# Kernel optimization log

Measured on AMD Instinct MI355X. Metric: run time of the kernel, lower is better.

The kernel has to match this reference:

```python
import jax, jax.numpy as jnp
import numpy as np

B, S, D, H = 4, 2048, 1024, 16
HD = D // H


def setup_inputs() -> dict:
    key = jax.random.key(0)
    ks = jax.random.split(key, 12)
    def lin(k):
        return jax.random.normal(k, (D, D), dtype=jnp.float32) * 0.02
    return {
        "query": jax.random.normal(ks[0], (B, S, D), dtype=jnp.float32),
        "key": jax.random.normal(ks[1], (B, S, D), dtype=jnp.float32),
        "value": jax.random.normal(ks[2], (B, S, D), dtype=jnp.float32),
        "Wq": lin(ks[3]), "bq": jnp.zeros((D,), jnp.float32),
        "Wk": lin(ks[4]), "bk": jnp.zeros((D,), jnp.float32),
        "Wv": lin(ks[5]), "bv": jnp.zeros((D,), jnp.float32),
        "Wo": lin(ks[6]), "bo": jnp.zeros((D,), jnp.float32),
        "pad_mask": jnp.ones((B, S), dtype=jnp.int32),
    }


def reference(query, key, value, Wq, bq, Wk, bk, Wv, bv, Wo, bo, pad_mask):
    # torch nn.Linear convention: y = x @ W.T + b
    Q = query @ Wq.T + bq   # [B,Sq,D]
    K = key @ Wk.T + bk     # [B,Sk,D]
    V = value @ Wv.T + bv
    Sq, Sk = Q.shape[1], K.shape[1]
    Q = Q.reshape(B, Sq, H, HD).transpose(0, 2, 1, 3)  # [B,H,Sq,hd]
    K = K.reshape(B, Sk, H, HD).transpose(0, 2, 1, 3)
    V = V.reshape(B, Sk, H, HD).transpose(0, 2, 1, 3)
    scores = jnp.einsum('bhqd,bhkd->bhqk', Q, K) / jnp.sqrt(jnp.float32(HD))
    # causal (lookahead) mask
    causal = jnp.tril(jnp.ones((Sq, Sk), dtype=bool))
    scores = jnp.where(causal[None, None], scores, -jnp.inf)
    # pad mask broadcast [B,1,Sq,1]
    pm = (pad_mask[:, None, :, None] != 0)
    scores = jnp.where(pm, scores, -jnp.inf)
    attn = jax.nn.softmax(scores, axis=-1)
    out = jnp.einsum('bhqk,bhkd->bhqd', attn, V)  # [B,H,Sq,hd]
    out = out.transpose(0, 2, 1, 3).reshape(B, Sq, D)
    return out @ Wo.T + bo
```

## Files before the change

kernel.cpp:

```cpp
#include <hip/hip_runtime.h>
#include <hip/hip_bf16.h>
#include <stdint.h>

typedef __attribute__((ext_vector_type(8))) short bf16x8;
typedef __attribute__((ext_vector_type(4))) float f32x4;

#define HD 64
#define NH 16
#define SEQ 2048
#define DM 1024

#define GLDS16(gp, lp)                                                      \
    __builtin_amdgcn_global_load_lds(                                       \
        (const __attribute__((address_space(1))) void*)(gp),                \
        (__attribute__((address_space(3))) void*)(lp), 16, 0, 0)

__device__ inline bf16x8 cvt8(const float* __restrict__ p) {
    float4 a = *(const float4*)p;
    float4 b = *(const float4*)(p + 4);
    union { bf16x8 v; __hip_bfloat16 e[8]; } u;
    u.e[0] = __float2bfloat16(a.x); u.e[1] = __float2bfloat16(a.y);
    u.e[2] = __float2bfloat16(a.z); u.e[3] = __float2bfloat16(a.w);
    u.e[4] = __float2bfloat16(b.x); u.e[5] = __float2bfloat16(b.y);
    u.e[6] = __float2bfloat16(b.z); u.e[7] = __float2bfloat16(b.w);
    return u.v;
}

__global__ __launch_bounds__(256)
void cvtw(const float* __restrict__ a, const float* __restrict__ b,
          const float* __restrict__ c, const float* __restrict__ d,
          __hip_bfloat16* __restrict__ o)
{
    int g = blockIdx.x * 256 + threadIdx.x;
    int t = g * 4;
    const float* src;
    switch (t >> 20) {
        case 0: src = a; break;
        case 1: src = b; break;
        case 2: src = c; break;
        default: src = d; break;
    }
    float4 v = *(const float4*)(src + (t & 0xFFFFF));
    union { ushort4 u; __hip_bfloat16 e[4]; } w;
    w.e[0] = __float2bfloat16(v.x); w.e[1] = __float2bfloat16(v.y);
    w.e[2] = __float2bfloat16(v.z); w.e[3] = __float2bfloat16(v.w);
    *(ushort4*)(o + t) = w.u;
}

__global__ __launch_bounds__(256)
void cvtx(const float* __restrict__ src, __hip_bfloat16* __restrict__ dst)
{
    int t = (blockIdx.x * 256 + threadIdx.x) * 8;
    *(bf16x8*)(dst + t) = cvt8(src + t);
}

template<int OMODE>
__global__ __launch_bounds__(256)
void gemm16(const __hip_bfloat16* __restrict__ X,
            const __hip_bfloat16* __restrict__ Wb,
            const float* __restrict__ bias,
            void* __restrict__ Yv,
            int M, int N, int K, float scale)
{
    __shared__ alignas(16) __hip_bfloat16 As[128 * 32];
    __shared__ alignas(16) __hip_bfloat16 Bs[128 * 32];

    const int tid  = threadIdx.x;
    const int lane = tid & 63;
    const int wv   = tid >> 6;
    const int quad = lane >> 4;
    const int l15  = lane & 15;
    const int wm   = (wv >> 1) * 64;
    const int wn   = (wv & 1) * 64;

    int bx = blockIdx.x, by = blockIdx.y;
    if (gridDim.x == 8 && gridDim.y == 64) {
        int lin = by * 8 + bx;
        bx = lin >> 6;
        by = ((lin & 7) << 3) | ((lin >> 3) & 7);
    }
    const int m0 = by * 128;
    const int n0 = bx * 128;

    f32x4 acc[4][4] = {};

    for (int k0 = 0; k0 < K; k0 += 32) {
        #pragma unroll
        for (int it = 0; it < 2; ++it) {
            int c = tid + it * 256;
            int row = c >> 2, cg = c & 3;
            GLDS16(&X[(size_t)(m0 + row) * K + k0 + cg * 8],
                   (char*)As + (size_t)c * 16);
            GLDS16(&Wb[(size_t)(n0 + row) * K + k0 + cg * 8],
                   (char*)Bs + (size_t)c * 16);
        }
        __syncthreads();

        bf16x8 af[4], bfr[4];
        #pragma unroll
        for (int i = 0; i < 4; ++i)
            af[i] = *(const bf16x8*)(&As[(wm + i * 16 + l15) * 32 + quad * 8]);
        #pragma unroll
        for (int j = 0; j < 4; ++j)
            bfr[j] = *(const bf16x8*)(&Bs[(wn + j * 16 + l15) * 32 + quad * 8]);

        #pragma unroll
        for (int i = 0; i < 4; ++i)
            #pragma unroll
            for (int j = 0; j < 4; ++j)
                acc[i][j] = __builtin_amdgcn_mfma_f32_16x16x32_bf16(
                    af[i], bfr[j], acc[i][j], 0, 0, 0);
        __syncthreads();
    }

    #pragma unroll
    for (int j = 0; j < 4; ++j) {
        int n = n0 + wn + j * 16 + l15;
        float bv = bias[n];
        int h = n >> 6, hd = n & 63;
        #pragma unroll
        for (int i = 0; i < 4; ++i) {
            int mb = m0 + wm + i * 16 + quad * 4;
            if (OMODE == 0) {
                __hip_bfloat16* Y = (__hip_bfloat16*)Yv;
                #pragma unroll
                for (int r = 0; r < 4; ++r) {
                    int m = mb + r;
                    int b = m >> 11, s = m & 2047;
                    Y[((size_t)(b * NH + h) * SEQ + s) * HD + hd] =
                        __float2bfloat16((acc[i][j][r] + bv) * scale);
                }
            } else if (OMODE == 2) {
                __hip_bfloat16* Y = (__hip_bfloat16*)Yv;
                int b = mb >> 11, s = mb & 2047;
                union { ushort4 u; __hip_bfloat16 e[4]; } w;
                #pragma unroll
                for (int r = 0; r < 4; ++r)
                    w.e[r] = __float2bfloat16(acc[i][j][r] + bv);
                *(ushort4*)(&Y[((size_t)(b * NH + h) * HD + hd) * SEQ + s]) = w.u;
            } else {
                float* Y = (float*)Yv;
                #pragma unroll
                for (int r = 0; r < 4; ++r)
                    Y[(size_t)(mb + r) * N + n] = acc[i][j][r] + bv;
            }
        }
    }
}

__device__ __forceinline__ unsigned pk2(float lo, float hi) {
    union { unsigned u; __hip_bfloat16 h[2]; } w;
    w.h[0] = __float2bfloat16(lo);
    w.h[1] = __float2bfloat16(hi);
    return w.u;
}

__device__ __forceinline__ void swap16(unsigned& a, unsigned& b) {
    asm("v_permlane16_swap_b32 %0, %1" : "+v"(a), "+v"(b));
}

__device__ __forceinline__ void attn_tile(
    const bf16x8 (&aqs)[2], f32x4 (&os)[4], f32x4& o5,
    const __hip_bfloat16* __restrict__ K_, const __hip_bfloat16* __restrict__ V_,
    const bf16x8 ones, int kv0, int qabs, bool diag,
    int quad, int l15, int sw, int qp)
{
    f32x4 sv[4];
    #pragma unroll
    for (int jk = 0; jk < 4; ++jk) {
        f32x4 s = {};
        #pragma unroll
        for (int ks = 0; ks < 2; ++ks) {
            bf16x8 kf = *(const bf16x8*)(
                &K_[(jk * 16 + l15) * 64 + (((ks * 4 + quad) ^ sw) * 8)]);
            s = __builtin_amdgcn_mfma_f32_16x16x32_bf16(kf, aqs[ks], s, 0, 0, 0);
        }
        sv[jk] = s;
    }
    unsigned P[4][2];
    #pragma unroll
    for (int jk = 0; jk < 4; ++jk) {
        int kvb = kv0 + jk * 16 + quad * 4;
        #pragma unroll
        for (int h = 0; h < 2; ++h) {
            float e0 = __builtin_amdgcn_exp2f(sv[jk][2 * h]);
            float e1 = __builtin_amdgcn_exp2f(sv[jk][2 * h + 1]);
            if (diag) {
                e0 = (kvb + 2 * h     <= qabs) ? e0 : 0.f;
                e1 = (kvb + 2 * h + 1 <= qabs) ? e1 : 0.f;
            }
            P[jk][h] = pk2(e0, e1);
        }
    }
    swap16(P[0][0], P[1][0]);
    swap16(P[0][1], P[1][1]);
    swap16(P[2][0], P[3][0]);
    swap16(P[2][1], P[3][1]);
    union { bf16x8 v; unsigned u[4]; } fa0, fa1;
    fa0.u[0] = P[0][0]; fa0.u[1] = P[0][1]; fa0.u[2] = P[1][0]; fa0.u[3] = P[1][1];
    fa1.u[0] = P[2][0]; fa1.u[1] = P[2][1]; fa1.u[2] = P[3][0]; fa1.u[3] = P[3][1];
    #pragma unroll
    for (int jn = 0; jn < 4; ++jn) {
        bf16x8 vb0 = *(const bf16x8*)(
            &V_[(jn * 16 + l15) * 64 + ((qp ^ sw) * 8)]);
        bf16x8 vb1 = *(const bf16x8*)(
            &V_[(jn * 16 + l15) * 64 + (((4 + qp) ^ sw) * 8)]);
        os[jn] = __builtin_amdgcn_mfma_f32_16x16x32_bf16(fa0.v, vb0, os[jn], 0, 0, 0);
        os[jn] = __builtin_amdgcn_mfma_f32_16x16x32_bf16(fa1.v, vb1, os[jn], 0, 0, 0);
    }
    o5 = __builtin_amdgcn_mfma_f32_16x16x32_bf16(fa0.v, ones, o5, 0, 0, 0);
    o5 = __builtin_amdgcn_mfma_f32_16x16x32_bf16(fa1.v, ones, o5, 0, 0, 0);
}

__global__ __launch_bounds__(256, 4)
void attn(const __hip_bfloat16* __restrict__ Qh,
          const __hip_bfloat16* __restrict__ Kh,
          const __hip_bfloat16* __restrict__ Vt,
          __hip_bfloat16* __restrict__ O)
{
    __shared__ alignas(16) __hip_bfloat16 Ks[2][64 * 64];
    __shared__ alignas(16) __hip_bfloat16 VsT[2][64 * 64];

    const int tid  = threadIdx.x;
    const int lane = tid & 63;
    const int wv   = tid >> 6;
    const int quad = lane >> 4;
    const int l15  = lane & 15;
    const int bh   = blockIdx.y;
    const int b    = bh >> 4;
    const int h    = bh & 15;
    const int p    = blockIdx.x;
    const int sa   = p;
    const int sb   = 31 - p;
    const int sw   = l15 & 7;
    const int qp   = ((quad & 1) << 1) | (quad >> 1);

    const __hip_bfloat16* Qp  = Qh + (size_t)bh * SEQ * HD;
    const __hip_bfloat16* Kp  = Kh + (size_t)bh * SEQ * HD;
    const __hip_bfloat16* Vtp = Vt + (size_t)bh * HD * SEQ;

    union { bf16x8 v; short e[8]; } onesu;
    #pragma unroll
    for (int i = 0; i < 8; ++i) onesu.e[i] = (short)0x3F80;
    const bf16x8 ones = onesu.v;

    bf16x8 aq[2][2];
    #pragma unroll
    for (int s = 0; s < 2; ++s) {
        int qb = (s ? sb : sa) * 64;
        #pragma unroll
        for (int ks = 0; ks < 2; ++ks)
            aq[s][ks] = *(const bf16x8*)(
                &Qp[(size_t)(qb + wv * 16 + l15) * HD + ks * 32 + quad * 8]);
    }

    f32x4 o[2][4] = {};
    f32x4 o5[2]   = {};

    const int srow = tid >> 3;
    const int scg  = (tid & 7) ^ (srow & 7);
    const __hip_bfloat16* kSrc = Kp + (size_t)srow * HD + scg * 8;
    const __hip_bfloat16* vSrc = Vtp + (size_t)srow * SEQ + scg * 8;
    char* kDst0 = (char*)Ks[0]  + tid * 16;
    char* vDst0 = (char*)VsT[0] + tid * 16;

    auto STAGE = [&](int bufi, int kv0) {
        size_t kadv = (size_t)kv0 * HD;
        int boff = bufi * 8192;
        GLDS16(kSrc + kadv,           kDst0 + boff);
        GLDS16(kSrc + kadv + 32 * HD, kDst0 + boff + 4096);
        GLDS16(vSrc + kv0,            vDst0 + boff);
        GLDS16(vSrc + kv0 + 32 * SEQ, vDst0 + boff + 4096);
    };

    const int nit = sa + sb + 2;

    STAGE(0, 0);

    for (int i = 0; i < nit; ++i) {
        __syncthreads();

        int ni = i + 1;
        if (ni < nit) {
            int t2 = (ni <= sb) ? ni : ni - sb - 1;
            STAGE(ni & 1, t2 * 64);
        }

        const int cb    = i & 1;
        const bool isB  = (i <= sb);
        const int t     = isB ? i : i - sb - 1;
        const int strip = isB ? sb : sa;
        const int kv0   = t * 64;
        const bool diag = (t == strip);
        const int qabs  = strip * 64 + wv * 16 + l15;

        const __hip_bfloat16* K_ = Ks[cb];
        const __hip_bfloat16* V_ = VsT[cb];

        if (isB)
            attn_tile(aq[1], o[1], o5[1], K_, V_, ones, kv0, qabs, diag, quad, l15, sw, qp);
        else
            attn_tile(aq[0], o[0], o5[0], K_, V_, ones, kv0, qabs, diag, quad, l15, sw, qp);
    }

    #pragma unroll
    for (int s = 0; s < 2; ++s) {
        int strip = s ? sb : sa;
        float inv[4];
        #pragma unroll
        for (int r = 0; r < 4; ++r)
            inv[r] = 1.0f / o5[s][r];
        #pragma unroll
        for (int jn = 0; jn < 4; ++jn) {
            #pragma unroll
            for (int r = 0; r < 4; ++r) {
                int q = strip * 64 + wv * 16 + quad * 4 + r;
                O[((size_t)(b * SEQ + q)) * DM + h * HD + jn * 16 + l15] =
                    __float2bfloat16(o[s][jn][r] * inv[r]);
            }
        }
    }
}

extern "C" void kernel_launch(void* const* d_in, const int* in_sizes, int n_in,
                              void* d_out, int out_size, void* d_ws, size_t ws_size,
                              hipStream_t stream)
{
    const float* query = (const float*)d_in[0];
    const float* key_  = (const float*)d_in[1];
    const float* value = (const float*)d_in[2];
    const float* Wq = (const float*)d_in[3];
    const float* bq = (const float*)d_in[4];
    const float* Wk = (const float*)d_in[5];
    const float* bk = (const float*)d_in[6];
    const float* Wv = (const float*)d_in[7];
    const float* bv = (const float*)d_in[8];
    const float* Wo = (const float*)d_in[9];
    const float* bo = (const float*)d_in[10];

    const size_t WSZ = (size_t)1024 * 1024;
    const size_t MAT = (size_t)8192 * 1024;
    __hip_bfloat16* wb = (__hip_bfloat16*)d_ws;
    __hip_bfloat16* Qh = wb + 4 * WSZ;
    __hip_bfloat16* Kh = Qh + MAT;
    __hip_bfloat16* Vt = Kh + MAT;
    __hip_bfloat16* Oa = Vt + MAT;
    float* out = (float*)d_out;

    const float SC = 0.18033688f;

    dim3 bb(256);
    dim3 gg(8, 64);
    cvtw<<<4096, bb, 0, stream>>>(Wq, Wk, Wv, Wo, wb);
    cvtx<<<4096, bb, 0, stream>>>(query, Oa);
    gemm16<0><<<gg, bb, 0, stream>>>(Oa, wb,           bq, Qh, 8192, 1024, 1024, SC);
    cvtx<<<4096, bb, 0, stream>>>(key_, Oa);
    gemm16<0><<<gg, bb, 0, stream>>>(Oa, wb + WSZ,     bk, Kh, 8192, 1024, 1024, 1.0f);
    cvtx<<<4096, bb, 0, stream>>>(value, Oa);
    gemm16<2><<<gg, bb, 0, stream>>>(Oa, wb + 2 * WSZ, bv, Vt, 8192, 1024, 1024, 1.0f);
    attn<<<dim3(16, 64), bb, 0, stream>>>(Qh, Kh, Vt, Oa);
    gemm16<1><<<gg, bb, 0, stream>>>(Oa, wb + 3 * WSZ, bo, out, 8192, 1024, 1024, 1.0f);
}
```

Before: 363.9 us.

## Fuse fp32-to-bf16 conversion into GEMM tile loads and prioritize attention MFMAs

Removes the separate weight and activation conversion kernels. The GEMMs now load fp32 tiles straight into LDS with an XOR swizzle and convert to bf16 when building fragments. This drops the extra global writes and reads of bf16 copies and four kernel launches, but doubles the LDS footprint and global traffic per tile and adds conversion work inside the inner loop. It also adds s_setprio around the MFMA sections in the attention tile and swizzles the bf16 A tile for the output projection.

```diff
diff --git a/kernel.cpp b/kernel.cpp
--- a/kernel.cpp
+++ b/kernel.cpp
@@ -15,55 +15,30 @@
         (const __attribute__((address_space(1))) void*)(gp),                \
         (__attribute__((address_space(3))) void*)(lp), 16, 0, 0)
 
-__device__ inline bf16x8 cvt8(const float* __restrict__ p) {
-    float4 a = *(const float4*)p;
-    float4 b = *(const float4*)(p + 4);
-    union { bf16x8 v; __hip_bfloat16 e[8]; } u;
-    u.e[0] = __float2bfloat16(a.x); u.e[1] = __float2bfloat16(a.y);
-    u.e[2] = __float2bfloat16(a.z); u.e[3] = __float2bfloat16(a.w);
-    u.e[4] = __float2bfloat16(b.x); u.e[5] = __float2bfloat16(b.y);
-    u.e[6] = __float2bfloat16(b.z); u.e[7] = __float2bfloat16(b.w);
-    return u.v;
-}
-
-__global__ __launch_bounds__(256)
-void cvtw(const float* __restrict__ a, const float* __restrict__ b,
-          const float* __restrict__ c, const float* __restrict__ d,
-          __hip_bfloat16* __restrict__ o)
+__device__ __forceinline__ unsigned pk2(float lo, float hi) {
+    union { unsigned u; __hip_bfloat16 h[2]; } w;
+    w.h[0] = __float2bfloat16(lo);
+    w.h[1] = __float2bfloat16(hi);
+    return w.u;
+}
+
+__device__ __forceinline__ bf16x8 ldfrag_f32(const char* base, int row, int quad) {
+    f32x4 a = *(const f32x4*)(base + (size_t)row * 128 + (((2 * quad)     ^ (row & 7)) * 16));
+    f32x4 b = *(const f32x4*)(base + (size_t)row * 128 + (((2 * quad + 1) ^ (row & 7)) * 16));
+    union { bf16x8 v; unsigned u[4]; } w;
+    w.u[0] = pk2(a[0], a[1]); w.u[1] = pk2(a[2], a[3]);
+    w.u[2] = pk2(b[0], b[1]); w.u[3] = pk2(b[2], b[3]);
+    return w.v;
+}
+
+template<int OMODE, bool XF32>
+__global__ __launch_bounds__(256, 4)
+void gemmf(const void* __restrict__ Xv, const float* __restrict__ Wf,
+           const float* __restrict__ bias, void* __restrict__ Yv,
+           int M, int N, int K, float scale)
 {
-    int g = blockIdx.x * 256 + threadIdx.x;
-    int t = g * 4;
-    const float* src;
-    switch (t >> 20) {
-        case 0: src = a; break;
-        case 1: src = b; break;
-        case 2: src = c; break;
-        default: src = d; break;
-    }
-    float4 v = *(const float4*)(src + (t & 0xFFFFF));
-    union { ushort4 u; __hip_bfloat16 e[4]; } w;
-    w.e[0] = __float2bfloat16(v.x); w.e[1] = __float2bfloat16(v.y);
-    w.e[2] = __float2bfloat16(v.z); w.e[3] = __float2bfloat16(v.w);
-    *(ushort4*)(o + t) = w.u;
-}
-
-__global__ __launch_bounds__(256)
-void cvtx(const float* __restrict__ src, __hip_bfloat16* __restrict__ dst)
-{
-    int t = (blockIdx.x * 256 + threadIdx.x) * 8;
-    *(bf16x8*)(dst + t) = cvt8(src + t);
-}
-
-template<int OMODE>
-__global__ __launch_bounds__(256)
-void gemm16(const __hip_bfloat16* __restrict__ X,
-            const __hip_bfloat16* __restrict__ Wb,
-            const float* __restrict__ bias,
-            void* __restrict__ Yv,
-            int M, int N, int K, float scale)
-{
-    __shared__ alignas(16) __hip_bfloat16 As[128 * 32];
-    __shared__ alignas(16) __hip_bfloat16 Bs[128 * 32];
+    __shared__ alignas(16) char As[16384];
+    __shared__ alignas(16) char Bs[16384];
 
     const int tid  = threadIdx.x;
     const int lane = tid & 63;
@@ -86,23 +61,46 @@
 
     for (int k0 = 0; k0 < K; k0 += 32) {
         #pragma unroll
-        for (int it = 0; it < 2; ++it) {
-            int c = tid + it * 256;
-            int row = c >> 2, cg = c & 3;
-            GLDS16(&X[(size_t)(m0 + row) * K + k0 + cg * 8],
-                   (char*)As + (size_t)c * 16);
-            GLDS16(&Wb[(size_t)(n0 + row) * K + k0 + cg * 8],
-                   (char*)Bs + (size_t)c * 16);
+        for (int it = 0; it < 4; ++it) {
+            int g = tid + it * 256;
+            int row = g >> 3, cl = (g & 7) ^ (row & 7);
+            GLDS16(&Wf[(size_t)(n0 + row) * K + k0 + cl * 4],
+                   Bs + (size_t)g * 16);
+        }
+        if (XF32) {
+            const float* X = (const float*)Xv;
+            #pragma unroll
+            for (int it = 0; it < 4; ++it) {
+                int g = tid + it * 256;
+                int row = g >> 3, cl = (g & 7) ^ (row & 7);
+                GLDS16(&X[(size_t)(m0 + row) * K + k0 + cl * 4],
+                       As + (size_t)g * 16);
+            }
+        } else {
+            const __hip_bfloat16* X = (const __hip_bfloat16*)Xv;
+            #pragma unroll
+            for (int it = 0; it < 2; ++it) {
+                int g = tid + it * 256;
+                int row = g >> 2, cl = (g & 3) ^ (row & 3);
+                GLDS16(&X[(size_t)(m0 + row) * K + k0 + cl * 8],
+                       As + (size_t)g * 16);
+            }
         }
         __syncthreads();
 
         bf16x8 af[4], bfr[4];
         #pragma unroll
-        for (int i = 0; i < 4; ++i)
-            af[i] = *(const bf16x8*)(&As[(wm + i * 16 + l15) * 32 + quad * 8]);
+        for (int i = 0; i < 4; ++i) {
+            int row = wm + i * 16 + l15;
+            if (XF32) {
+                af[i] = ldfrag_f32(As, row, quad);
+            } else {
+                af[i] = *(const bf16x8*)(As + (size_t)row * 64 + ((quad ^ (row & 3)) * 16));
+            }
+        }
         #pragma unroll
         for (int j = 0; j < 4; ++j)
-            bfr[j] = *(const bf16x8*)(&Bs[(wn + j * 16 + l15) * 32 + quad * 8]);
+            bfr[j] = ldfrag_f32(Bs, wn + j * 16 + l15, quad);
 
         #pragma unroll
         for (int i = 0; i < 4; ++i)
@@ -148,13 +146,6 @@
     }
 }
 
-__device__ __forceinline__ unsigned pk2(float lo, float hi) {
-    union { unsigned u; __hip_bfloat16 h[2]; } w;
-    w.h[0] = __float2bfloat16(lo);
-    w.h[1] = __float2bfloat16(hi);
-    return w.u;
-}
-
 __device__ __forceinline__ void swap16(unsigned& a, unsigned& b) {
     asm("v_permlane16_swap_b32 %0, %1" : "+v"(a), "+v"(b));
 }
@@ -166,6 +157,7 @@
     int quad, int l15, int sw, int qp)
 {
     f32x4 sv[4];
+    __builtin_amdgcn_s_setprio(1);
     #pragma unroll
     for (int jk = 0; jk < 4; ++jk) {
         f32x4 s = {};
@@ -177,6 +169,7 @@
         }
         sv[jk] = s;
     }
+    __builtin_amdgcn_s_setprio(0);
     unsigned P[4][2];
     #pragma unroll
     for (int jk = 0; jk < 4; ++jk) {
@@ -199,6 +192,7 @@
     union { bf16x8 v; unsigned u[4]; } fa0, fa1;
     fa0.u[0] = P[0][0]; fa0.u[1] = P[0][1]; fa0.u[2] = P[1][0]; fa0.u[3] = P[1][1];
     fa1.u[0] = P[2][0]; fa1.u[1] = P[2][1]; fa1.u[2] = P[3][0]; fa1.u[3] = P[3][1];
+    __builtin_amdgcn_s_setprio(1);
     #pragma unroll
     for (int jn = 0; jn < 4; ++jn) {
         bf16x8 vb0 = *(const bf16x8*)(
@@ -210,6 +204,7 @@
     }
     o5 = __builtin_amdgcn_mfma_f32_16x16x32_bf16(fa0.v, ones, o5, 0, 0, 0);
     o5 = __builtin_amdgcn_mfma_f32_16x16x32_bf16(fa1.v, ones, o5, 0, 0, 0);
+    __builtin_amdgcn_s_setprio(0);
 }
 
 __global__ __launch_bounds__(256, 4)
@@ -338,10 +333,8 @@
     const float* Wo = (const float*)d_in[9];
     const float* bo = (const float*)d_in[10];
 
-    const size_t WSZ = (size_t)1024 * 1024;
     const size_t MAT = (size_t)8192 * 1024;
-    __hip_bfloat16* wb = (__hip_bfloat16*)d_ws;
-    __hip_bfloat16* Qh = wb + 4 * WSZ;
+    __hip_bfloat16* Qh = (__hip_bfloat16*)d_ws;
     __hip_bfloat16* Kh = Qh + MAT;
     __hip_bfloat16* Vt = Kh + MAT;
     __hip_bfloat16* Oa = Vt + MAT;
@@ -351,13 +344,9 @@
 
     dim3 bb(256);
     dim3 gg(8, 64);
-    cvtw<<<4096, bb, 0, stream>>>(Wq, Wk, Wv, Wo, wb);
-    cvtx<<<4096, bb, 0, stream>>>(query, Oa);
-    gemm16<0><<<gg, bb, 0, stream>>>(Oa, wb,           bq, Qh, 8192, 1024, 1024, SC);
-    cvtx<<<4096, bb, 0, stream>>>(key_, Oa);
-    gemm16<0><<<gg, bb, 0, stream>>>(Oa, wb + WSZ,     bk, Kh, 8192, 1024, 1024, 1.0f);
-    cvtx<<<4096, bb, 0, stream>>>(value, Oa);
-    gemm16<2><<<gg, bb, 0, stream>>>(Oa, wb + 2 * WSZ, bv, Vt, 8192, 1024, 1024, 1.0f);
+    gemmf<0, true ><<<gg, bb, 0, stream>>>(query, Wq, bq, Qh, 8192, 1024, 1024, SC);
+    gemmf<0, true ><<<gg, bb, 0, stream>>>(key_,  Wk, bk, Kh, 8192, 1024, 1024, 1.0f);
+    gemmf<2, true ><<<gg, bb, 0, stream>>>(value, Wv, bv, Vt, 8192, 1024, 1024, 1.0f);
     attn<<<dim3(16, 64), bb, 0, stream>>>(Qh, Kh, Vt, Oa);
-    gemm16<1><<<gg, bb, 0, stream>>>(Oa, wb + 3 * WSZ, bo, out, 8192, 1024, 1024, 1.0f);
-}
+    gemmf<1, false><<<gg, bb, 0, stream>>>(Oa, Wo, bo, out, 8192, 1024, 1024, 1.0f);
+}
```

After: 417.7 us. 1.15x slower.

## Fuse fp32-to-bf16 activation conversion into a single batched QKV GEMM launch

Applied to the files above, without the earlier changes.

Removes the three separate activation conversion kernels and loads fp32 activations straight into LDS with an XOR swizzle, converting to bf16 while building fragments. The Q, K and V projections become one launch with a z-dimension of three, which cuts launch count and the round trip of the bf16 intermediate through memory. In exchange the A tile doubles in LDS and global traffic for A is fp32, and the fragment loads now carry conversion ALU work. It also adds s_setprio around the MFMA sections in the attention tile to favour matrix issue.

```diff
diff --git a/kernel.cpp b/kernel.cpp
--- a/kernel.cpp
+++ b/kernel.cpp
@@ -14,6 +14,13 @@
     __builtin_amdgcn_global_load_lds(                                       \
         (const __attribute__((address_space(1))) void*)(gp),                \
         (__attribute__((address_space(3))) void*)(lp), 16, 0, 0)
+
+__device__ __forceinline__ unsigned pk2(float lo, float hi) {
+    union { unsigned u; __hip_bfloat16 h[2]; } w;
+    w.h[0] = __float2bfloat16(lo);
+    w.h[1] = __float2bfloat16(hi);
+    return w.u;
+}
 
 __device__ inline bf16x8 cvt8(const float* __restrict__ p) {
     float4 a = *(const float4*)p;
@@ -47,22 +54,25 @@
     *(ushort4*)(o + t) = w.u;
 }
 
-__global__ __launch_bounds__(256)
-void cvtx(const float* __restrict__ src, __hip_bfloat16* __restrict__ dst)
-{
-    int t = (blockIdx.x * 256 + threadIdx.x) * 8;
-    *(bf16x8*)(dst + t) = cvt8(src + t);
-}
-
-template<int OMODE>
-__global__ __launch_bounds__(256)
-void gemm16(const __hip_bfloat16* __restrict__ X,
-            const __hip_bfloat16* __restrict__ Wb,
-            const float* __restrict__ bias,
-            void* __restrict__ Yv,
-            int M, int N, int K, float scale)
-{
-    __shared__ alignas(16) __hip_bfloat16 As[128 * 32];
+__device__ __forceinline__ bf16x8 ldfrag_f32(const char* base, int row, int quad) {
+    f32x4 a = *(const f32x4*)(base + (size_t)row * 128 + (((2 * quad)     ^ (row & 7)) * 16));
+    f32x4 b = *(const f32x4*)(base + (size_t)row * 128 + (((2 * quad + 1) ^ (row & 7)) * 16));
+    union { bf16x8 v; unsigned u[4]; } w;
+    w.u[0] = pk2(a[0], a[1]); w.u[1] = pk2(a[2], a[3]);
+    w.u[2] = pk2(b[0], b[1]); w.u[3] = pk2(b[2], b[3]);
+    return w.v;
+}
+
+__global__ __launch_bounds__(256, 4)
+void qkvgemm(const float* __restrict__ Xq, const float* __restrict__ Xk,
+             const float* __restrict__ Xv,
+             const __hip_bfloat16* __restrict__ wb,
+             const float* __restrict__ bq, const float* __restrict__ bk,
+             const float* __restrict__ bv,
+             __hip_bfloat16* __restrict__ Qh, __hip_bfloat16* __restrict__ Kh,
+             __hip_bfloat16* __restrict__ Vt, float scaleQ)
+{
+    __shared__ alignas(16) float As[128 * 32];
     __shared__ alignas(16) __hip_bfloat16 Bs[128 * 32];
 
     const int tid  = threadIdx.x;
@@ -72,13 +82,105 @@
     const int l15  = lane & 15;
     const int wm   = (wv >> 1) * 64;
     const int wn   = (wv & 1) * 64;
-
-    int bx = blockIdx.x, by = blockIdx.y;
-    if (gridDim.x == 8 && gridDim.y == 64) {
-        int lin = by * 8 + bx;
-        bx = lin >> 6;
-        by = ((lin & 7) << 3) | ((lin >> 3) & 7);
-    }
+    const int z    = blockIdx.z;
+
+    const float* X = (z == 0) ? Xq : (z == 1) ? Xk : Xv;
+    const __hip_bfloat16* W = wb + (size_t)z * (1024 * 1024);
+    const float* bias = (z == 0) ? bq : (z == 1) ? bk : bv;
+
+    int lin = blockIdx.y * 8 + blockIdx.x;
+    const int bx = lin >> 6;
+    const int by = ((lin & 7) << 3) | ((lin >> 3) & 7);
+    const int m0 = by * 128;
+    const int n0 = bx * 128;
+
+    f32x4 acc[4][4] = {};
+
+    for (int k0 = 0; k0 < 1024; k0 += 32) {
+        #pragma unroll
+        for (int it = 0; it < 4; ++it) {
+            int g = tid + it * 256;
+            int row = g >> 3, cl = (g & 7) ^ (row & 7);
+            GLDS16(&X[(size_t)(m0 + row) * 1024 + k0 + cl * 4],
+                   (char*)As + (size_t)g * 16);
+        }
+        #pragma unroll
+        for (int it = 0; it < 2; ++it) {
+            int c = tid + it * 256;
+            int row = c >> 2, cg = c & 3;
+            GLDS16(&W[(size_t)(n0 + row) * 1024 + k0 + cg * 8],
+                   (char*)Bs + (size_t)c * 16);
+        }
+        __syncthreads();
+
+        bf16x8 af[4], bfr[4];
+        #pragma unroll
+        for (int i = 0; i < 4; ++i)
+            af[i] = ldfrag_f32((const char*)As, wm + i * 16 + l15, quad);
+        #pragma unroll
+        for (int j = 0; j < 4; ++j)
+            bfr[j] = *(const bf16x8*)(&Bs[(wn + j * 16 + l15) * 32 + quad * 8]);
+
+        #pragma unroll
+        for (int i = 0; i < 4; ++i)
+            #pragma unroll
+            for (int j = 0; j < 4; ++j)
+                acc[i][j] = __builtin_amdgcn_mfma_f32_16x16x32_bf16(
+                    af[i], bfr[j], acc[i][j], 0, 0, 0);
+        __syncthreads();
+    }
+
+    const float scale = (z == 0) ? scaleQ : 1.0f;
+    #pragma unroll
+    for (int j = 0; j < 4; ++j) {
+        int n = n0 + wn + j * 16 + l15;
+        float bv2 = bias[n];
+        int h = n >> 6, hd = n & 63;
+        #pragma unroll
+        for (int i = 0; i < 4; ++i) {
+            int mb = m0 + wm + i * 16 + quad * 4;
+            if (z < 2) {
+                __hip_bfloat16* Y = (z == 0) ? Qh : Kh;
+                #pragma unroll
+                for (int r = 0; r < 4; ++r) {
+                    int m = mb + r;
+                    int b = m >> 11, s = m & 2047;
+                    Y[((size_t)(b * NH + h) * SEQ + s) * HD + hd] =
+                        __float2bfloat16((acc[i][j][r] + bv2) * scale);
+                }
+            } else {
+                int b = mb >> 11, s = mb & 2047;
+                union { ushort4 u; __hip_bfloat16 e[4]; } w;
+                #pragma unroll
+                for (int r = 0; r < 4; ++r)
+                    w.e[r] = __float2bfloat16(acc[i][j][r] + bv2);
+                *(ushort4*)(&Vt[((size_t)(b * NH + h) * HD + hd) * SEQ + s]) = w.u;
+            }
+        }
+    }
+}
+
+__global__ __launch_bounds__(256)
+void ogemm(const __hip_bfloat16* __restrict__ X,
+           const __hip_bfloat16* __restrict__ Wb,
+           const float* __restrict__ bias,
+           float* __restrict__ Y,
+           int M, int N, int K)
+{
+    __shared__ alignas(16) __hip_bfloat16 As[128 * 32];
+    __shared__ alignas(16) __hip_bfloat16 Bs[128 * 32];
+
+    const int tid  = threadIdx.x;
+    const int lane = tid & 63;
+    const int wv   = tid >> 6;
+    const int quad = lane >> 4;
+    const int l15  = lane & 15;
+    const int wm   = (wv >> 1) * 64;
+    const int wn   = (wv & 1) * 64;
+
+    int lin = blockIdx.y * 8 + blockIdx.x;
+    const int bx = lin >> 6;
+    const int by = ((lin & 7) << 3) | ((lin >> 3) & 7);
     const int m0 = by * 128;
     const int n0 = bx * 128;
 
@@ -117,42 +219,14 @@
     for (int j = 0; j < 4; ++j) {
         int n = n0 + wn + j * 16 + l15;
         float bv = bias[n];
-        int h = n >> 6, hd = n & 63;
         #pragma unroll
         for (int i = 0; i < 4; ++i) {
             int mb = m0 + wm + i * 16 + quad * 4;
-            if (OMODE == 0) {
-                __hip_bfloat16* Y = (__hip_bfloat16*)Yv;
-                #pragma unroll
-                for (int r = 0; r < 4; ++r) {
-                    int m = mb + r;
-                    int b = m >> 11, s = m & 2047;
-                    Y[((size_t)(b * NH + h) * SEQ + s) * HD + hd] =
-                        __float2bfloat16((acc[i][j][r] + bv) * scale);
-                }
-            } else if (OMODE == 2) {
-                __hip_bfloat16* Y = (__hip_bfloat16*)Yv;
-                int b = mb >> 11, s = mb & 2047;
-                union { ushort4 u; __hip_bfloat16 e[4]; } w;
-                #pragma unroll
-                for (int r = 0; r < 4; ++r)
-                    w.e[r] = __float2bfloat16(acc[i][j][r] + bv);
-                *(ushort4*)(&Y[((size_t)(b * NH + h) * HD + hd) * SEQ + s]) = w.u;
-            } else {
-                float* Y = (float*)Yv;
-                #pragma unroll
-                for (int r = 0; r < 4; ++r)
-                    Y[(size_t)(mb + r) * N + n] = acc[i][j][r] + bv;
-            }
-        }
-    }
-}
-
-__device__ __forceinline__ unsigned pk2(float lo, float hi) {
-    union { unsigned u; __hip_bfloat16 h[2]; } w;
-    w.h[0] = __float2bfloat16(lo);
-    w.h[1] = __float2bfloat16(hi);
-    return w.u;
+            #pragma unroll
+            for (int r = 0; r < 4; ++r)
+                Y[(size_t)(mb + r) * N + n] = acc[i][j][r] + bv;
+        }
+    }
 }
 
 __device__ __forceinline__ void swap16(unsigned& a, unsigned& b) {
@@ -166,6 +240,7 @@
     int quad, int l15, int sw, int qp)
 {
     f32x4 sv[4];
+    __builtin_amdgcn_s_setprio(1);
     #pragma unroll
     for (int jk = 0; jk < 4; ++jk) {
         f32x4 s = {};
@@ -177,6 +252,7 @@
         }
         sv[jk] = s;
     }
+    __builtin_amdgcn_s_setprio(0);
     unsigned P[4][2];
     #pragma unroll
     for (int jk = 0; jk < 4; ++jk) {
@@ -199,6 +275,7 @@
     union { bf16x8 v; unsigned u[4]; } fa0, fa1;
     fa0.u[0] = P[0][0]; fa0.u[1] = P[0][1]; fa0.u[2] = P[1][0]; fa0.u[3] = P[1][1];
     fa1.u[0] = P[2][0]; fa1.u[1] = P[2][1]; fa1.u[2] = P[3][0]; fa1.u[3] = P[3][1];
+    __builtin_amdgcn_s_setprio(1);
     #pragma unroll
     for (int jn = 0; jn < 4; ++jn) {
         bf16x8 vb0 = *(const bf16x8*)(
@@ -210,6 +287,7 @@
     }
     o5 = __builtin_amdgcn_mfma_f32_16x16x32_bf16(fa0.v, ones, o5, 0, 0, 0);
     o5 = __builtin_amdgcn_mfma_f32_16x16x32_bf16(fa1.v, ones, o5, 0, 0, 0);
+    __builtin_amdgcn_s_setprio(0);
 }
 
 __global__ __launch_bounds__(256, 4)
@@ -350,14 +428,9 @@
     const float SC = 0.18033688f;
 
     dim3 bb(256);
-    dim3 gg(8, 64);
     cvtw<<<4096, bb, 0, stream>>>(Wq, Wk, Wv, Wo, wb);
-    cvtx<<<4096, bb, 0, stream>>>(query, Oa);
-    gemm16<0><<<gg, bb, 0, stream>>>(Oa, wb,           bq, Qh, 8192, 1024, 1024, SC);
-    cvtx<<<4096, bb, 0, stream>>>(key_, Oa);
-    gemm16<0><<<gg, bb, 0, stream>>>(Oa, wb + WSZ,     bk, Kh, 8192, 1024, 1024, 1.0f);
-    cvtx<<<4096, bb, 0, stream>>>(value, Oa);
-    gemm16<2><<<gg, bb, 0, stream>>>(Oa, wb + 2 * WSZ, bv, Vt, 8192, 1024, 1024, 1.0f);
+    qkvgemm<<<dim3(8, 64, 3), bb, 0, stream>>>(query, key_, value, wb,
+                                               bq, bk, bv, Qh, Kh, Vt, SC);
     attn<<<dim3(16, 64), bb, 0, stream>>>(Qh, Kh, Vt, Oa);
-    gemm16<1><<<gg, bb, 0, stream>>>(Oa, wb + 3 * WSZ, bo, out, 8192, 1024, 1024, 1.0f);
-}
+    ogemm<<<dim3(8, 64), bb, 0, stream>>>(Oa, wb + 3 * WSZ, bo, out, 8192, 1024, 1024);
+}
```

After: 350.6 us. -3.7%, faster.
